# Kernel optimization log

Hardware: AMD Instinct MI355X
Metric: run time of the kernel (lower is better)

The kernel has to match this reference:

```python
import jax, jax.numpy as jnp
import numpy as np

H_BINS = 64
SIGMA = 0.02
EPS = 1e-6


def setup_inputs() -> dict:
    key = jax.random.key(0)
    x = jax.random.uniform(key, (8, 3, 256, 256), dtype=jnp.float32)
    return {"x": x}


def reference(x):
    h = H_BINS
    L = x.shape[0]
    x = jnp.clip(x, 0.0, 1.0)
    I = x.reshape(L, 3, -1)                      # [L,3,N]
    Iy = jnp.sqrt(jnp.sum(I * I, axis=1) + EPS)  # [L,N] pixel intensity
    logs = jnp.log(I + EPS)                      # [L,3,N]
    # per-channel log-chromaticity: for c=0:(u=l0-l1, v=l0-l2); c=1:(l1-l0, l1-l2); c=2:(l2-l0, l2-l1)
    cu = jnp.array([1, 0, 0])
    cv = jnp.array([2, 2, 1])
    U = logs - logs[:, cu, :]                    # [L,3,N]
    V = logs - logs[:, cv, :]                    # [L,3,N]
    offset = jnp.linspace(-3.0, 3.0, h, dtype=jnp.float32)  # [h]
    inv_s2 = jnp.float32(1.0 / (SIGMA * SIGMA))
    # RBF-like (inverse-quadratic) soft binning kernels: [L,3,N,h]
    Ku = 1.0 / (1.0 + jnp.square(U[..., None] - offset) * inv_s2)
    Kv = 1.0 / (1.0 + jnp.square(V[..., None] - offset) * inv_s2)
    # weighted outer-product reduction over pixels -> [L,3,h,h]
    hists = jnp.einsum('ln,lcnu,lcnv->lcuv', Iy, Ku, Kv)
    # normalize each sample by its total mass
    total = jnp.sum(hists, axis=(1, 2, 3), keepdims=True)
    return hists / (total + EPS)
```

## Files before the change

kernel.cpp:

```cpp
#include <hip/hip_runtime.h>

#define H 64
#define NPIX 65536
#define LBATCH 8
#define LC 24
#define S_CHUNKS 32
#define PB 2048
#define EPSF 1e-6f
#define LN2_50 34.6573590f

#define WS_PART ((size_t)S_CHUNKS * LC * H * H)
#define NEED_WS ((WS_PART + LC * 16) * 4)

typedef _Float16 h8 __attribute__((ext_vector_type(8)));
typedef _Float16 h4 __attribute__((ext_vector_type(4)));
typedef _Float16 h2 __attribute__((ext_vector_type(2)));
typedef short    s2 __attribute__((ext_vector_type(2)));
typedef float f32x16 __attribute__((ext_vector_type(16)));
union H8p { h8 v8; h2 h[4]; };

#if __has_builtin(__builtin_elementwise_fma)
#define FMA2(a, b, c) __builtin_elementwise_fma((a), (b), (c))
#else
#define FMA2(a, b, c) ((a) * (b) + (c))
#endif

static __device__ __forceinline__ h2 kev2(h2 u2, h2 o2, h2 one2, h2 two2,
                                          h2 clamp2, s2 magic2) {
    const h2 d  = u2 - o2;
    const h2 xx = __builtin_elementwise_min(FMA2(d, d, one2), clamp2);
    h2 y = __builtin_bit_cast(h2, (s2)(magic2 - __builtin_bit_cast(s2, xx)));
    y = y * FMA2(-xx, y, two2);
    y = y * FMA2(-xx, y, two2);
    return y;
}

__global__ __launch_bounds__(256) void hist_zero(float* __restrict__ out) {
    out[blockIdx.x * 256 + threadIdx.x] = 0.0f;
}

__global__ __launch_bounds__(256, 2) void hist_main(const float* __restrict__ x,
                                                    float* __restrict__ dst,
                                                    int atomic_mode) {
    __shared__ _Float16 sUh[PB];
    __shared__ _Float16 sVh[PB];
    __shared__ _Float16 sWh[PB];
    __shared__ float sHist[H * H];

    const int tid  = threadIdx.x;
    const int wv   = tid >> 6;
    const int lane = tid & 63;
    const int hf   = lane >> 5;
    const int ln   = lane & 31;
    const int lc   = blockIdx.y;
    const int l    = lc / 3;
    const int c    = lc - 3 * l;

    #pragma unroll
    for (int r = 0; r < 4; r++)
        *(float4*)&sHist[(r * 256 + tid) * 4] = make_float4(0.f, 0.f, 0.f, 0.f);

    const float* __restrict__ x0p = x + (l * 3 + 0) * NPIX;
    const float* __restrict__ x1p = x + (l * 3 + 1) * NPIX;
    const float* __restrict__ x2p = x + (l * 3 + 2) * NPIX;
    const int base = blockIdx.x * PB;

    #pragma unroll
    for (int pass = 0; pass < 2; pass++) {
        const int ploc = pass * 1024 + tid * 4;
        const float4 r0 = *(const float4*)&x0p[base + ploc];
        const float4 r1 = *(const float4*)&x1p[base + ploc];
        const float4 r2 = *(const float4*)&x2p[base + ploc];
        float4 U4, V4, W4;
        #define PREP(E) { \
            const float v0 = fminf(fmaxf(r0.E, 0.0f), 1.0f); \
            const float v1 = fminf(fmaxf(r1.E, 0.0f), 1.0f); \
            const float v2 = fminf(fmaxf(r2.E, 0.0f), 1.0f); \
            W4.E = __builtin_amdgcn_sqrtf(fmaf(v0, v0, fmaf(v1, v1, fmaf(v2, v2, EPSF)))); \
            const float lg0 = __builtin_amdgcn_logf(v0 + EPSF); \
            const float lg1 = __builtin_amdgcn_logf(v1 + EPSF); \
            const float lg2 = __builtin_amdgcn_logf(v2 + EPSF); \
            float U, V; \
            if (c == 0)      { U = lg0 - lg1; V = lg0 - lg2; } \
            else if (c == 1) { U = lg1 - lg0; V = lg1 - lg2; } \
            else             { U = lg2 - lg0; V = lg2 - lg1; } \
            U4.E = LN2_50 * U; V4.E = LN2_50 * V; }
        PREP(x) PREP(y) PREP(z) PREP(w)
        #undef PREP
        *(h4*)&sUh[ploc] = h4{(_Float16)U4.x, (_Float16)U4.y, (_Float16)U4.z, (_Float16)U4.w};
        *(h4*)&sVh[ploc] = h4{(_Float16)V4.x, (_Float16)V4.y, (_Float16)V4.z, (_Float16)V4.w};
        *(h4*)&sWh[ploc] = h4{(_Float16)W4.x, (_Float16)W4.y, (_Float16)W4.z, (_Float16)W4.w};
    }
    __syncthreads();

    const float step50 = 50.0f * (6.0f / 63.0f);
    const float ou0 = -150.0f + step50 * (float)ln;
    const float ou1 = ou0 + step50 * 32.0f;
    const h2 o0_2 = {(_Float16)ou0, (_Float16)ou0};
    const h2 o1_2 = {(_Float16)ou1, (_Float16)ou1};
    const h2 one2   = {(_Float16)1.0f, (_Float16)1.0f};
    const h2 two2   = {(_Float16)2.0f, (_Float16)2.0f};
    const h2 clamp2 = {(_Float16)16384.0f, (_Float16)16384.0f};
    const s2 magic2 = {(short)0x779A, (short)0x779A};

    f32x16 acc00, acc01, acc10, acc11;
    #pragma unroll
    for (int i = 0; i < 16; i++) { acc00[i] = 0.f; acc01[i] = 0.f; acc10[i] = 0.f; acc11[i] = 0.f; }

    const int wbase = wv * 512;
    #pragma unroll 4
    for (int ks = 0; ks < 32; ks++) {
        const int kb = wbase + ks * 16 + hf * 8;
        H8p U, V, W, A0, A1, B0, B1;
        U.v8 = *(const h8*)&sUh[kb];
        V.v8 = *(const h8*)&sVh[kb];
        W.v8 = *(const h8*)&sWh[kb];
        #pragma unroll
        for (int q = 0; q < 4; q++) {
            A0.h[q] = W.h[q] * kev2(U.h[q], o0_2, one2, two2, clamp2, magic2);
            A1.h[q] = W.h[q] * kev2(U.h[q], o1_2, one2, two2, clamp2, magic2);
            B0.h[q] = kev2(V.h[q], o0_2, one2, two2, clamp2, magic2);
            B1.h[q] = kev2(V.h[q], o1_2, one2, two2, clamp2, magic2);
        }
        acc00 = __builtin_amdgcn_mfma_f32_32x32x16_f16(A0.v8, B0.v8, acc00, 0, 0, 0);
        acc01 = __builtin_amdgcn_mfma_f32_32x32x16_f16(A0.v8, B1.v8, acc01, 0, 0, 0);
        acc10 = __builtin_amdgcn_mfma_f32_32x32x16_f16(A1.v8, B0.v8, acc10, 0, 0, 0);
        acc11 = __builtin_amdgcn_mfma_f32_32x32x16_f16(A1.v8, B1.v8, acc11, 0, 0, 0);
    }

    #pragma unroll
    for (int r = 0; r < 16; r++) {
        const int row = (r & 3) + 8 * (r >> 2) + 4 * hf;
        atomicAdd(&sHist[row * 64 + ln],             acc00[r]);
        atomicAdd(&sHist[row * 64 + 32 + ln],        acc01[r]);
        atomicAdd(&sHist[(row + 32) * 64 + ln],      acc10[r]);
        atomicAdd(&sHist[(row + 32) * 64 + 32 + ln], acc11[r]);
    }
    __syncthreads();

    if (atomic_mode == 0) {
        float* __restrict__ g = dst + (blockIdx.x * LC + lc) * (H * H);
        #pragma unroll
        for (int r = 0; r < 4; r++) {
            const int i = (r * 256 + tid) * 4;
            *(float4*)&g[i] = *(const float4*)&sHist[i];
        }
    } else {
        float* __restrict__ g = dst + lc * (H * H);
        #pragma unroll
        for (int r = 0; r < 16; r++) {
            const int i = r * 256 + tid;
            unsafeAtomicAdd(&g[i], sHist[i]);
        }
    }
}

__global__ __launch_bounds__(256) void hist_reduce(const float* __restrict__ part,
                                                   float* __restrict__ out,
                                                   float* __restrict__ sums) {
    const int lc  = blockIdx.x >> 4;
    const int seg = blockIdx.x & 15;
    const int i   = lc * (H * H) + seg * 256 + threadIdx.x;
    float s = 0.0f;
    #pragma unroll
    for (int sc = 0; sc < S_CHUNKS; sc++)
        s += part[sc * (LC * H * H) + i];
    out[i] = s;
    float t = s;
    #pragma unroll
    for (int off = 32; off > 0; off >>= 1) t += __shfl_down(t, off, 64);
    __shared__ float ps[4];
    if ((threadIdx.x & 63) == 0) ps[threadIdx.x >> 6] = t;
    __syncthreads();
    if (threadIdx.x == 0) sums[blockIdx.x] = (ps[0] + ps[1]) + (ps[2] + ps[3]);
}

__global__ __launch_bounds__(256) void hist_norm(float* __restrict__ out,
                                                 const float* __restrict__ sums) {
    const int i = blockIdx.x * 256 + threadIdx.x;
    const int l = blockIdx.x / 48;
    float T = 0.0f;
    #pragma unroll
    for (int k = 0; k < 48; k++) T += sums[l * 48 + k];
    out[i] = out[i] / (T + EPSF);
}

__global__ __launch_bounds__(256) void hist_finish(float* __restrict__ out) {
    const int l = blockIdx.x;
    float* __restrict__ p = out + l * 3 * H * H;
    float s = 0.0f;
    #pragma unroll
    for (int it = 0; it < 12; it++) {
        const float4 v = *(const float4*)&p[(it * 256 + threadIdx.x) * 4];
        s += (v.x + v.y) + (v.z + v.w);
    }
    #pragma unroll
    for (int off = 32; off > 0; off >>= 1) s += __shfl_down(s, off, 64);
    __shared__ float ps[4];
    if ((threadIdx.x & 63) == 0) ps[threadIdx.x >> 6] = s;
    __syncthreads();
    const float T = (ps[0] + ps[1]) + (ps[2] + ps[3]);
    const float inv = 1.0f / (T + EPSF);
    #pragma unroll
    for (int it = 0; it < 12; it++) {
        float4 v = *(const float4*)&p[(it * 256 + threadIdx.x) * 4];
        v.x *= inv; v.y *= inv; v.z *= inv; v.w *= inv;
        *(float4*)&p[(it * 256 + threadIdx.x) * 4] = v;
    }
}

extern "C" void kernel_launch(void* const* d_in, const int* in_sizes, int n_in,
                              void* d_out, int out_size, void* d_ws, size_t ws_size,
                              hipStream_t stream) {
    const float* x = (const float*)d_in[0];
    float* out = (float*)d_out;
    float* ws  = (float*)d_ws;

    if (ws_size >= NEED_WS) {
        float* sums = ws + WS_PART;
        hipLaunchKernelGGL(hist_main,   dim3(S_CHUNKS, LC),      dim3(256), 0, stream, x, ws, 0);
        hipLaunchKernelGGL(hist_reduce, dim3(LC * 16),           dim3(256), 0, stream, ws, out, sums);
        hipLaunchKernelGGL(hist_norm,   dim3(LC * H * H / 256),  dim3(256), 0, stream, out, sums);
    } else {
        hipLaunchKernelGGL(hist_zero,   dim3(LC * H * H / 256), dim3(256), 0, stream, out);
        hipLaunchKernelGGL(hist_main,   dim3(S_CHUNKS, LC),     dim3(256), 0, stream, x, out, 1);
        hipLaunchKernelGGL(hist_finish, dim3(LBATCH),           dim3(256), 0, stream, out);
    }
}
```

Before: 152.6 us.

## Share log-chromaticity kernels across channels via sign-flip symmetry of offsets

```diff
diff --git a/kernel.cpp b/kernel.cpp
--- a/kernel.cpp
+++ b/kernel.cpp
@@ -4,12 +4,12 @@
 #define NPIX 65536
 #define LBATCH 8
 #define LC 24
-#define S_CHUNKS 32
-#define PB 2048
+#define S_CHUNKS 64
+#define PB 1024
 #define EPSF 1e-6f
 #define LN2_50 34.6573590f
 
-#define WS_PART ((size_t)S_CHUNKS * LC * H * H)
+#define WS_PART ((size_t)LBATCH * S_CHUNKS * 3 * H * H)
 #define NEED_WS ((WS_PART + LC * 16) * 4)
 
 typedef _Float16 h8 __attribute__((ext_vector_type(8)));
@@ -35,43 +35,44 @@
     return y;
 }
 
+#define MFMA(a, b, acc) __builtin_amdgcn_mfma_f32_32x32x16_f16((a), (b), (acc), 0, 0, 0)
+
 __global__ __launch_bounds__(256) void hist_zero(float* __restrict__ out) {
     out[blockIdx.x * 256 + threadIdx.x] = 0.0f;
 }
 
-__global__ __launch_bounds__(256, 2) void hist_main(const float* __restrict__ x,
+__global__ __launch_bounds__(256, 1) void hist_main(const float* __restrict__ x,
                                                     float* __restrict__ dst,
                                                     int atomic_mode) {
-    __shared__ _Float16 sUh[PB];
-    __shared__ _Float16 sVh[PB];
-    __shared__ _Float16 sWh[PB];
-    __shared__ float sHist[H * H];
+    __shared__ _Float16 sD01[PB];
+    __shared__ _Float16 sD02[PB];
+    __shared__ _Float16 sD12[PB];
+    __shared__ _Float16 sWw[PB];
+    __shared__ float sH[3 * H * H];
 
     const int tid  = threadIdx.x;
     const int wv   = tid >> 6;
     const int lane = tid & 63;
     const int hf   = lane >> 5;
     const int ln   = lane & 31;
-    const int lc   = blockIdx.y;
-    const int l    = lc / 3;
-    const int c    = lc - 3 * l;
-
-    #pragma unroll
-    for (int r = 0; r < 4; r++)
-        *(float4*)&sHist[(r * 256 + tid) * 4] = make_float4(0.f, 0.f, 0.f, 0.f);
+    const int l    = blockIdx.y;
+    const int chnk = blockIdx.x;
+
+    #pragma unroll
+    for (int r = 0; r < 12; r++)
+        *(float4*)&sH[(r * 256 + tid) * 4] = make_float4(0.f, 0.f, 0.f, 0.f);
 
     const float* __restrict__ x0p = x + (l * 3 + 0) * NPIX;
     const float* __restrict__ x1p = x + (l * 3 + 1) * NPIX;
     const float* __restrict__ x2p = x + (l * 3 + 2) * NPIX;
-    const int base = blockIdx.x * PB;
-
-    #pragma unroll
-    for (int pass = 0; pass < 2; pass++) {
-        const int ploc = pass * 1024 + tid * 4;
+    const int base = chnk * PB;
+
+    {
+        const int ploc = tid * 4;
         const float4 r0 = *(const float4*)&x0p[base + ploc];
         const float4 r1 = *(const float4*)&x1p[base + ploc];
         const float4 r2 = *(const float4*)&x2p[base + ploc];
-        float4 U4, V4, W4;
+        float4 A4, B4, C4, W4;
         #define PREP(E) { \
             const float v0 = fminf(fmaxf(r0.E, 0.0f), 1.0f); \
             const float v1 = fminf(fmaxf(r1.E, 0.0f), 1.0f); \
@@ -80,16 +81,15 @@
             const float lg0 = __builtin_amdgcn_logf(v0 + EPSF); \
             const float lg1 = __builtin_amdgcn_logf(v1 + EPSF); \
             const float lg2 = __builtin_amdgcn_logf(v2 + EPSF); \
-            float U, V; \
-            if (c == 0)      { U = lg0 - lg1; V = lg0 - lg2; } \
-            else if (c == 1) { U = lg1 - lg0; V = lg1 - lg2; } \
-            else             { U = lg2 - lg0; V = lg2 - lg1; } \
-            U4.E = LN2_50 * U; V4.E = LN2_50 * V; }
+            A4.E = LN2_50 * (lg0 - lg1); \
+            B4.E = LN2_50 * (lg0 - lg2); \
+            C4.E = LN2_50 * (lg1 - lg2); }
         PREP(x) PREP(y) PREP(z) PREP(w)
         #undef PREP
-        *(h4*)&sUh[ploc] = h4{(_Float16)U4.x, (_Float16)U4.y, (_Float16)U4.z, (_Float16)U4.w};
-        *(h4*)&sVh[ploc] = h4{(_Float16)V4.x, (_Float16)V4.y, (_Float16)V4.z, (_Float16)V4.w};
-        *(h4*)&sWh[ploc] = h4{(_Float16)W4.x, (_Float16)W4.y, (_Float16)W4.z, (_Float16)W4.w};
+        *(h4*)&sD01[ploc] = h4{(_Float16)A4.x, (_Float16)A4.y, (_Float16)A4.z, (_Float16)A4.w};
+        *(h4*)&sD02[ploc] = h4{(_Float16)B4.x, (_Float16)B4.y, (_Float16)B4.z, (_Float16)B4.w};
+        *(h4*)&sD12[ploc] = h4{(_Float16)C4.x, (_Float16)C4.y, (_Float16)C4.z, (_Float16)C4.w};
+        *(h4*)&sWw[ploc]  = h4{(_Float16)W4.x, (_Float16)W4.y, (_Float16)W4.z, (_Float16)W4.w};
     }
     __syncthreads();
 
@@ -103,54 +103,97 @@
     const h2 clamp2 = {(_Float16)16384.0f, (_Float16)16384.0f};
     const s2 magic2 = {(short)0x779A, (short)0x779A};
 
-    f32x16 acc00, acc01, acc10, acc11;
-    #pragma unroll
-    for (int i = 0; i < 16; i++) { acc00[i] = 0.f; acc01[i] = 0.f; acc10[i] = 0.f; acc11[i] = 0.f; }
-
-    const int wbase = wv * 512;
-    #pragma unroll 4
-    for (int ks = 0; ks < 32; ks++) {
-        const int kb = wbase + ks * 16 + hf * 8;
-        H8p U, V, W, A0, A1, B0, B1;
-        U.v8 = *(const h8*)&sUh[kb];
-        V.v8 = *(const h8*)&sVh[kb];
-        W.v8 = *(const h8*)&sWh[kb];
+    f32x16 g0_00, g0_01, g0_10, g0_11;
+    f32x16 g1_00, g1_01, g1_10, g1_11;
+    f32x16 g2_00, g2_01, g2_10, g2_11;
+    #pragma unroll
+    for (int i = 0; i < 16; i++) {
+        g0_00[i] = 0.f; g0_01[i] = 0.f; g0_10[i] = 0.f; g0_11[i] = 0.f;
+        g1_00[i] = 0.f; g1_01[i] = 0.f; g1_10[i] = 0.f; g1_11[i] = 0.f;
+        g2_00[i] = 0.f; g2_01[i] = 0.f; g2_10[i] = 0.f; g2_11[i] = 0.f;
+    }
+
+    const int wbase = wv * 256;
+    H8p d01, d02, d12, ww;
+    {
+        const int kb = wbase + hf * 8;
+        d01.v8 = *(const h8*)&sD01[kb];
+        d02.v8 = *(const h8*)&sD02[kb];
+        d12.v8 = *(const h8*)&sD12[kb];
+        ww.v8  = *(const h8*)&sWw[kb];
+    }
+    #pragma unroll 1
+    for (int ks = 0; ks < 16; ks++) {
+        const int kbn = wbase + ((ks + 1) & 15) * 16 + hf * 8;
+        H8p n01, n02, n12, nww;
+        n01.v8 = *(const h8*)&sD01[kbn];
+        n02.v8 = *(const h8*)&sD02[kbn];
+        n12.v8 = *(const h8*)&sD12[kbn];
+        nww.v8 = *(const h8*)&sWw[kbn];
+
+        H8p a01t0, a01t1, b02t0, b02t1, a02t0, a02t1, b12t0, b12t1;
         #pragma unroll
         for (int q = 0; q < 4; q++) {
-            A0.h[q] = W.h[q] * kev2(U.h[q], o0_2, one2, two2, clamp2, magic2);
-            A1.h[q] = W.h[q] * kev2(U.h[q], o1_2, one2, two2, clamp2, magic2);
-            B0.h[q] = kev2(V.h[q], o0_2, one2, two2, clamp2, magic2);
-            B1.h[q] = kev2(V.h[q], o1_2, one2, two2, clamp2, magic2);
+            const h2 k01t0 = kev2(d01.h[q], o0_2, one2, two2, clamp2, magic2);
+            const h2 k01t1 = kev2(d01.h[q], o1_2, one2, two2, clamp2, magic2);
+            a01t0.h[q] = ww.h[q] * k01t0;
+            a01t1.h[q] = ww.h[q] * k01t1;
+            b02t0.h[q] = kev2(d02.h[q], o0_2, one2, two2, clamp2, magic2);
+            b02t1.h[q] = kev2(d02.h[q], o1_2, one2, two2, clamp2, magic2);
+            a02t0.h[q] = ww.h[q] * b02t0.h[q];
+            a02t1.h[q] = ww.h[q] * b02t1.h[q];
+            b12t0.h[q] = kev2(d12.h[q], o0_2, one2, two2, clamp2, magic2);
+            b12t1.h[q] = kev2(d12.h[q], o1_2, one2, two2, clamp2, magic2);
         }
-        acc00 = __builtin_amdgcn_mfma_f32_32x32x16_f16(A0.v8, B0.v8, acc00, 0, 0, 0);
-        acc01 = __builtin_amdgcn_mfma_f32_32x32x16_f16(A0.v8, B1.v8, acc01, 0, 0, 0);
-        acc10 = __builtin_amdgcn_mfma_f32_32x32x16_f16(A1.v8, B0.v8, acc10, 0, 0, 0);
-        acc11 = __builtin_amdgcn_mfma_f32_32x32x16_f16(A1.v8, B1.v8, acc11, 0, 0, 0);
+        g0_00 = MFMA(a01t0.v8, b02t0.v8, g0_00);
+        g0_01 = MFMA(a01t0.v8, b02t1.v8, g0_01);
+        g0_10 = MFMA(a01t1.v8, b02t0.v8, g0_10);
+        g0_11 = MFMA(a01t1.v8, b02t1.v8, g0_11);
+        g1_00 = MFMA(a01t0.v8, b12t0.v8, g1_00);
+        g1_01 = MFMA(a01t0.v8, b12t1.v8, g1_01);
+        g1_10 = MFMA(a01t1.v8, b12t0.v8, g1_10);
+        g1_11 = MFMA(a01t1.v8, b12t1.v8, g1_11);
+        g2_00 = MFMA(a02t0.v8, b12t0.v8, g2_00);
+        g2_01 = MFMA(a02t0.v8, b12t1.v8, g2_01);
+        g2_10 = MFMA(a02t1.v8, b12t0.v8, g2_10);
+        g2_11 = MFMA(a02t1.v8, b12t1.v8, g2_11);
+        d01 = n01; d02 = n02; d12 = n12; ww = nww;
     }
 
     #pragma unroll
     for (int r = 0; r < 16; r++) {
         const int row = (r & 3) + 8 * (r >> 2) + 4 * hf;
-        atomicAdd(&sHist[row * 64 + ln],             acc00[r]);
-        atomicAdd(&sHist[row * 64 + 32 + ln],        acc01[r]);
-        atomicAdd(&sHist[(row + 32) * 64 + ln],      acc10[r]);
-        atomicAdd(&sHist[(row + 32) * 64 + 32 + ln], acc11[r]);
+        float* __restrict__ h0 = &sH[0];
+        float* __restrict__ h1 = &sH[H * H];
+        float* __restrict__ h2s = &sH[2 * H * H];
+        atomicAdd(&h0[row * 64 + ln],              g0_00[r]);
+        atomicAdd(&h0[row * 64 + 32 + ln],         g0_01[r]);
+        atomicAdd(&h0[(row + 32) * 64 + ln],       g0_10[r]);
+        atomicAdd(&h0[(row + 32) * 64 + 32 + ln],  g0_11[r]);
+        atomicAdd(&h1[(63 - row) * 64 + ln],             g1_00[r]);
+        atomicAdd(&h1[(63 - row) * 64 + 32 + ln],        g1_01[r]);
+        atomicAdd(&h1[(31 - row) * 64 + ln],             g1_10[r]);
+        atomicAdd(&h1[(31 - row) * 64 + 32 + ln],        g1_11[r]);
+        atomicAdd(&h2s[(63 - row) * 64 + (63 - ln)],     g2_00[r]);
+        atomicAdd(&h2s[(63 - row) * 64 + (31 - ln)],     g2_01[r]);
+        atomicAdd(&h2s[(31 - row) * 64 + (63 - ln)],     g2_10[r]);
+        atomicAdd(&h2s[(31 - row) * 64 + (31 - ln)],     g2_11[r]);
     }
     __syncthreads();
 
     if (atomic_mode == 0) {
-        float* __restrict__ g = dst + (blockIdx.x * LC + lc) * (H * H);
+        float* __restrict__ g = dst + (size_t)(l * S_CHUNKS + chnk) * 3 * H * H;
         #pragma unroll
-        for (int r = 0; r < 4; r++) {
+        for (int r = 0; r < 12; r++) {
             const int i = (r * 256 + tid) * 4;
-            *(float4*)&g[i] = *(const float4*)&sHist[i];
+            *(float4*)&g[i] = *(const float4*)&sH[i];
         }
     } else {
-        float* __restrict__ g = dst + lc * (H * H);
+        float* __restrict__ g = dst + (size_t)l * 3 * H * H;
         #pragma unroll
-        for (int r = 0; r < 16; r++) {
+        for (int r = 0; r < 12; r++) {
             const int i = r * 256 + tid;
-            unsafeAtomicAdd(&g[i], sHist[i]);
+            unsafeAtomicAdd(&g[i], sH[i]);
         }
     }
 }
@@ -160,15 +203,17 @@
                                                    float* __restrict__ sums) {
     const int lc  = blockIdx.x >> 4;
     const int seg = blockIdx.x & 15;
-    const int i   = lc * (H * H) + seg * 256 + threadIdx.x;
+    const int l   = lc / 3;
+    const int c   = lc - 3 * l;
+    const int off = seg * 256 + threadIdx.x;
     float s = 0.0f;
-    #pragma unroll
+    #pragma unroll 4
     for (int sc = 0; sc < S_CHUNKS; sc++)
-        s += part[sc * (LC * H * H) + i];
-    out[i] = s;
+        s += part[((size_t)(l * S_CHUNKS + sc) * 3 + c) * (H * H) + off];
+    out[lc * (H * H) + off] = s;
     float t = s;
     #pragma unroll
-    for (int off = 32; off > 0; off >>= 1) t += __shfl_down(t, off, 64);
+    for (int o = 32; o > 0; o >>= 1) t += __shfl_down(t, o, 64);
     __shared__ float ps[4];
     if ((threadIdx.x & 63) == 0) ps[threadIdx.x >> 6] = t;
     __syncthreads();
@@ -218,12 +263,12 @@
 
     if (ws_size >= NEED_WS) {
         float* sums = ws + WS_PART;
-        hipLaunchKernelGGL(hist_main,   dim3(S_CHUNKS, LC),      dim3(256), 0, stream, x, ws, 0);
+        hipLaunchKernelGGL(hist_main,   dim3(S_CHUNKS, LBATCH),  dim3(256), 0, stream, x, ws, 0);
         hipLaunchKernelGGL(hist_reduce, dim3(LC * 16),           dim3(256), 0, stream, ws, out, sums);
         hipLaunchKernelGGL(hist_norm,   dim3(LC * H * H / 256),  dim3(256), 0, stream, out, sums);
     } else {
-        hipLaunchKernelGGL(hist_zero,   dim3(LC * H * H / 256), dim3(256), 0, stream, out);
-        hipLaunchKernelGGL(hist_main,   dim3(S_CHUNKS, LC),     dim3(256), 0, stream, x, out, 1);
-        hipLaunchKernelGGL(hist_finish, dim3(LBATCH),           dim3(256), 0, stream, out);
-    }
-}
+        hipLaunchKernelGGL(hist_zero,   dim3(LC * H * H / 256),  dim3(256), 0, stream, out);
+        hipLaunchKernelGGL(hist_main,   dim3(S_CHUNKS, LBATCH),  dim3(256), 0, stream, x, out, 1);
+        hipLaunchKernelGGL(hist_finish, dim3(LBATCH),            dim3(256), 0, stream, out);
+    }
+}
```

After: 215.0 us. +40.8%, slower.

## Use 1024-thread blocks over 8192-pixel chunks to shrink partial histograms

Applied to the files above, without the earlier changes.

```diff
diff --git a/kernel.cpp b/kernel.cpp
--- a/kernel.cpp
+++ b/kernel.cpp
@@ -4,12 +4,12 @@
 #define NPIX 65536
 #define LBATCH 8
 #define LC 24
-#define S_CHUNKS 32
-#define PB 2048
+#define N_CHUNKS 8
+#define PB 8192
 #define EPSF 1e-6f
 #define LN2_50 34.6573590f
 
-#define WS_PART ((size_t)S_CHUNKS * LC * H * H)
+#define WS_PART ((size_t)N_CHUNKS * LC * H * H)
 #define NEED_WS ((WS_PART + LC * 16) * 4)
 
 typedef _Float16 h8 __attribute__((ext_vector_type(8)));
@@ -35,13 +35,15 @@
     return y;
 }
 
+#define MFMA(a, b, acc) __builtin_amdgcn_mfma_f32_32x32x16_f16((a), (b), (acc), 0, 0, 0)
+
 __global__ __launch_bounds__(256) void hist_zero(float* __restrict__ out) {
     out[blockIdx.x * 256 + threadIdx.x] = 0.0f;
 }
 
-__global__ __launch_bounds__(256, 2) void hist_main(const float* __restrict__ x,
-                                                    float* __restrict__ dst,
-                                                    int atomic_mode) {
+__global__ __launch_bounds__(1024) void hist_main(const float* __restrict__ x,
+                                                  float* __restrict__ dst,
+                                                  int atomic_mode) {
     __shared__ _Float16 sUh[PB];
     __shared__ _Float16 sVh[PB];
     __shared__ _Float16 sWh[PB];
@@ -56,9 +58,7 @@
     const int l    = lc / 3;
     const int c    = lc - 3 * l;
 
-    #pragma unroll
-    for (int r = 0; r < 4; r++)
-        *(float4*)&sHist[(r * 256 + tid) * 4] = make_float4(0.f, 0.f, 0.f, 0.f);
+    *(float4*)&sHist[tid * 4] = make_float4(0.f, 0.f, 0.f, 0.f);
 
     const float* __restrict__ x0p = x + (l * 3 + 0) * NPIX;
     const float* __restrict__ x1p = x + (l * 3 + 1) * NPIX;
@@ -67,7 +67,7 @@
 
     #pragma unroll
     for (int pass = 0; pass < 2; pass++) {
-        const int ploc = pass * 1024 + tid * 4;
+        const int ploc = pass * 4096 + tid * 4;
         const float4 r0 = *(const float4*)&x0p[base + ploc];
         const float4 r1 = *(const float4*)&x1p[base + ploc];
         const float4 r2 = *(const float4*)&x2p[base + ploc];
@@ -108,7 +108,7 @@
     for (int i = 0; i < 16; i++) { acc00[i] = 0.f; acc01[i] = 0.f; acc10[i] = 0.f; acc11[i] = 0.f; }
 
     const int wbase = wv * 512;
-    #pragma unroll 4
+    #pragma unroll 2
     for (int ks = 0; ks < 32; ks++) {
         const int kb = wbase + ks * 16 + hf * 8;
         H8p U, V, W, A0, A1, B0, B1;
@@ -122,10 +122,10 @@
             B0.h[q] = kev2(V.h[q], o0_2, one2, two2, clamp2, magic2);
             B1.h[q] = kev2(V.h[q], o1_2, one2, two2, clamp2, magic2);
         }
-        acc00 = __builtin_amdgcn_mfma_f32_32x32x16_f16(A0.v8, B0.v8, acc00, 0, 0, 0);
-        acc01 = __builtin_amdgcn_mfma_f32_32x32x16_f16(A0.v8, B1.v8, acc01, 0, 0, 0);
-        acc10 = __builtin_amdgcn_mfma_f32_32x32x16_f16(A1.v8, B0.v8, acc10, 0, 0, 0);
-        acc11 = __builtin_amdgcn_mfma_f32_32x32x16_f16(A1.v8, B1.v8, acc11, 0, 0, 0);
+        acc00 = MFMA(A0.v8, B0.v8, acc00);
+        acc01 = MFMA(A0.v8, B1.v8, acc01);
+        acc10 = MFMA(A1.v8, B0.v8, acc10);
+        acc11 = MFMA(A1.v8, B1.v8, acc11);
     }
 
     #pragma unroll
@@ -139,17 +139,13 @@
     __syncthreads();
 
     if (atomic_mode == 0) {
-        float* __restrict__ g = dst + (blockIdx.x * LC + lc) * (H * H);
+        float* __restrict__ g = dst + (size_t)(blockIdx.x * LC + lc) * (H * H);
+        *(float4*)&g[tid * 4] = *(const float4*)&sHist[tid * 4];
+    } else {
+        float* __restrict__ g = dst + (size_t)lc * (H * H);
         #pragma unroll
         for (int r = 0; r < 4; r++) {
-            const int i = (r * 256 + tid) * 4;
-            *(float4*)&g[i] = *(const float4*)&sHist[i];
-        }
-    } else {
-        float* __restrict__ g = dst + lc * (H * H);
-        #pragma unroll
-        for (int r = 0; r < 16; r++) {
-            const int i = r * 256 + tid;
+            const int i = r * 1024 + tid;
             unsafeAtomicAdd(&g[i], sHist[i]);
         }
     }
@@ -163,12 +159,12 @@
     const int i   = lc * (H * H) + seg * 256 + threadIdx.x;
     float s = 0.0f;
     #pragma unroll
-    for (int sc = 0; sc < S_CHUNKS; sc++)
-        s += part[sc * (LC * H * H) + i];
+    for (int sc = 0; sc < N_CHUNKS; sc++)
+        s += part[(size_t)sc * (LC * H * H) + i];
     out[i] = s;
     float t = s;
     #pragma unroll
-    for (int off = 32; off > 0; off >>= 1) t += __shfl_down(t, off, 64);
+    for (int o = 32; o > 0; o >>= 1) t += __shfl_down(t, o, 64);
     __shared__ float ps[4];
     if ((threadIdx.x & 63) == 0) ps[threadIdx.x >> 6] = t;
     __syncthreads();
@@ -218,12 +214,12 @@
 
     if (ws_size >= NEED_WS) {
         float* sums = ws + WS_PART;
-        hipLaunchKernelGGL(hist_main,   dim3(S_CHUNKS, LC),      dim3(256), 0, stream, x, ws, 0);
-        hipLaunchKernelGGL(hist_reduce, dim3(LC * 16),           dim3(256), 0, stream, ws, out, sums);
-        hipLaunchKernelGGL(hist_norm,   dim3(LC * H * H / 256),  dim3(256), 0, stream, out, sums);
+        hipLaunchKernelGGL(hist_main,   dim3(N_CHUNKS, LC),     dim3(1024), 0, stream, x, ws, 0);
+        hipLaunchKernelGGL(hist_reduce, dim3(LC * 16),          dim3(256),  0, stream, ws, out, sums);
+        hipLaunchKernelGGL(hist_norm,   dim3(LC * H * H / 256), dim3(256),  0, stream, out, sums);
     } else {
-        hipLaunchKernelGGL(hist_zero,   dim3(LC * H * H / 256), dim3(256), 0, stream, out);
-        hipLaunchKernelGGL(hist_main,   dim3(S_CHUNKS, LC),     dim3(256), 0, stream, x, out, 1);
-        hipLaunchKernelGGL(hist_finish, dim3(LBATCH),           dim3(256), 0, stream, out);
-    }
-}
+        hipLaunchKernelGGL(hist_zero,   dim3(LC * H * H / 256), dim3(256),  0, stream, out);
+        hipLaunchKernelGGL(hist_main,   dim3(N_CHUNKS, LC),     dim3(1024), 0, stream, x, out, 1);
+        hipLaunchKernelGGL(hist_finish, dim3(LBATCH),           dim3(256),  0, stream, out);
+    }
+}
```

New measurement: 177.8 us. +16.5%, slower.
